# Optimization experiments

Measured on AMD Instinct MI355X. Metric: run time of the kernel, lower is better.

The kernel has to match this reference:

```python
import jax, jax.numpy as jnp
import numpy as np
from jax import lax

PATCH_SIZE = 7
NEIGH_SIZE = 9
SIGMA = 2.0
EPS = 1e-05


def _gaussian_kernel(sigma, sz):
    mid = sz // 2
    ax = np.arange(sz) - mid
    g = np.exp(-(ax[:, None] ** 2 + ax[None, :] ** 2) / (2.0 * sigma ** 2)) / (2.0 * np.pi * sigma ** 2)
    return g.astype(np.float32)


KERNEL = jnp.asarray(_gaussian_kernel(SIGMA, PATCH_SIZE))[None, None]  # (1,1,7,7)

_half = NEIGH_SIZE // 2
SHIFTS = jnp.asarray(
    [(x, y) for x in range(-_half, NEIGH_SIZE - _half)
     for y in range(-_half, NEIGH_SIZE - _half) if (x, y) != (0, 0)],
    dtype=jnp.int32)  # (80, 2) — xshift outer loop, yshift inner, matching torch order
SHIFTS4 = jnp.asarray([(-1, 0), (1, 0), (0, -1), (0, 1)], dtype=jnp.int32)


def _translate(img, tx, ty):
    # Faithful to torch affine_grid + grid_sample(nearest, zeros, align_corners=False):
    # a 'translation' of tx in normalized coords samples input at pixel j + tx*W/2.
    # H, W even and tx, ty integers -> exact integer pixel shifts, zero padding.
    H, W = img.shape
    px = jnp.arange(W) + tx * (W // 2)
    py = jnp.arange(H) + ty * (H // 2)
    mask = ((py >= 0) & (py < H))[:, None] & ((px >= 0) & (px < W))[None, :]
    out = img[jnp.clip(py, 0, H - 1)[:, None], jnp.clip(px, 0, W - 1)[None, :]]
    return jnp.where(mask, out, jnp.zeros((), img.dtype))


def _blur(x):
    # x: (N, H, W); conv2d with gaussian kernel, stride 1, padding 3 (same for 7x7)
    y = lax.conv_general_dilated(x[:, None], KERNEL, (1, 1), [(3, 3), (3, 3)],
                                 dimension_numbers=('NCHW', 'OIHW', 'NCHW'))
    return y[:, 0]


def _dp_batch(img2d, shifts):
    # Dp for a batch of shifts: shift, diff, square, gaussian blur
    shifted = jax.vmap(lambda s: _translate(img2d, s[0], s[1]))(shifts)  # (N,H,W)
    return _blur((img2d[None] - shifted) ** 2)


def setup_inputs() -> dict:
    key = jax.random.key(0)
    k1, k2 = jax.random.split(key)
    image1 = jax.random.normal(k1, (1, 1, 1024, 1024), dtype=jnp.float32)
    image2 = jax.random.normal(k2, (1, 1, 1024, 1024), dtype=jnp.float32)
    return {"image1": image1, "image2": image2}


def reference(image1, image2):
    img1 = image1[0, 0]  # (H, W)
    img2 = image2[0, 0]
    H, W = img1.shape
    reduce_size = (PATCH_SIZE + NEIGH_SIZE - 2) // 2  # = 7
    # Vimg: average of 4 single-pixel-neighborhood Dp's on image1, + eps
    Vimg = _dp_batch(img1, SHIFTS4).sum(axis=0) / 4.0 + EPS  # (H, W)
    # 80-shift MIND responses on image2
    D2 = _dp_batch(img2, SHIFTS)  # (80, H, W)
    mind = jnp.exp(-D2 / Vimg[None])
    # torch slices: dim1 end index is (C - reduce_size) = 1-7 = -6 -> H-6;
    # dim2 end index is (H - reduce_size). Replicated exactly (H == W).
    out = mind[:, reduce_size:H + 1 - reduce_size, reduce_size:H - reduce_size]
    mx = jnp.max(out, axis=0)
    return jnp.mean(out / mx[None])
```

## Files before the change

### kernel.cpp

```cpp
#include <hip/hip_runtime.h>
#include <cmath>

#define IMG_W 1024
#define SROWS 22
#define SCOLS 70

struct GK { float gh[7]; float gv[7]; };

__device__ __forceinline__ float4 pointwise(const float* __restrict__ img1,
                                            const float* __restrict__ img2,
                                            int sr, int sc)
{
    const int srp = sr ^ 512;
    const int scp = sc ^ 512;
    const float a  = img2[sr  * IMG_W + sc ];
    const float b  = img2[sr  * IMG_W + scp];
    const float cc = img2[srp * IMG_W + sc ];
    const float d  = img2[srp * IMG_W + scp];
    const float u  = img1[sr  * IMG_W + sc ];
    const float ub = img1[sr  * IMG_W + scp];
    const float uc = img1[srp * IMG_W + sc ];
    const float a2 = a * a;
    const float tb = a - b, tc = a - cc, td = a - d;
    const float su = u - ub, sv = u - uc;
    float4 f;
    f.x = fmaf(tb, tb, -a2);
    f.y = fmaf(tc, tc, -a2);
    f.z = fmaf(td, td, -a2);
    f.w = fmaf(u, u + u, fmaf(su, su, sv * sv));
    return f;
}

__global__ __launch_bounds__(256)
void mind_tile(const float* __restrict__ img1, const float* __restrict__ img2,
               float* __restrict__ partials, GK gk)
{
    __shared__ float4 s1[SROWS * SCOLS];

    const int tx  = (int)threadIdx.x;
    const int ty  = (int)threadIdx.y;
    const int tid = ty * 64 + tx;
    const int bx  = (int)blockIdx.x ^ 7;
    const int by  = (int)blockIdx.y ^ 31;
    const int x0  = 7 + 64 * bx;
    const int y0  = 7 + 16 * by;

    #pragma unroll
    for (int k = 0; k < 6; ++k) {
        const int e = tid + 256 * k;
        if (e < SROWS * 64) {
            const int r = e >> 6, c = e & 63;
            const int sr = min(y0 - 3 + r, 1023);
            const int sc = min(x0 - 3 + c, 1023);
            s1[r * SCOLS + c] = pointwise(img1, img2, sr, sc);
        }
    }
    {
        const int r = tid >> 3, c6 = tid & 7;
        if (r < SROWS && c6 < 6) {
            const int sr = min(y0 - 3 + r, 1023);
            const int sc = min(x0 + 61 + c6, 1023);
            s1[r * SCOLS + 64 + c6] = pointwise(img1, img2, sr, sc);
        }
    }
    __syncthreads();

    const bool xs = (x0 - 3 <= 511) && (x0 + 66 >= 512);
    const bool ys = (y0 - 3 <= 511) && (y0 + 18 >= 512);
    const bool xok = (x0 + tx <= 1016);
    float tsum = 0.f;

    if (!xs && !ys) {
        float Px[4] = {0,0,0,0}, Py[4] = {0,0,0,0}, Pd[4] = {0,0,0,0}, V4[4] = {0,0,0,0};
        #pragma unroll
        for (int r = 0; r < 10; ++r) {
            const float4* __restrict__ row = &s1[(4 * ty + r) * SCOLS + tx];
            float hH = 0, hV = 0, hD = 0, hU = 0;
            #pragma unroll
            for (int kx = 0; kx < 7; ++kx) {
                const float4 g = row[kx];
                hH = fmaf(gk.gh[kx], g.x, hH);
                hV = fmaf(gk.gh[kx], g.y, hV);
                hD = fmaf(gk.gh[kx], g.z, hD);
                hU = fmaf(gk.gh[kx], g.w, hU);
            }
            #pragma unroll
            for (int o = 0; o < 4; ++o) {
                if (r - o >= 0 && r - o <= 6) {
                    const float g = gk.gv[r - o];
                    Px[o] = fmaf(g, hH, Px[o]);
                    Py[o] = fmaf(g, hV, Py[o]);
                    Pd[o] = fmaf(g, hD, Pd[o]);
                    V4[o] = fmaf(g, hU, V4[o]);
                }
            }
        }
        #pragma unroll
        for (int o = 0; o < 4; ++o) {
            const float V = fmaf(V4[o], 0.25f, 1e-5f);
            const float invV = 1.0f / V;
            float M = fminf(0.f, Px[o]);
            M = fminf(M, Py[o]); M = fminf(M, Pd[o]);
            const float pix = 77.f * __expf(M * invV)
                + __expf((M - Px[o]) * invV)
                + __expf((M - Py[o]) * invV)
                + __expf((M - Pd[o]) * invV);
            const bool ok = xok && (y0 + 4 * ty + o <= 1017);
            tsum += ok ? pix : 0.f;
        }
    } else {
        float glx[7], ghx[7];
        #pragma unroll
        for (int kx = 0; kx < 7; ++kx) {
            const bool lo = (((x0 - 3 + tx + kx) & 512) == 0);
            glx[kx] = lo ? gk.gh[kx] : 0.f;
            ghx[kx] = lo ? 0.f : gk.gh[kx];
        }
        float Ph[4]  = {0,0,0,0}, Qh[4]  = {0,0,0,0}, Pv[4] = {0,0,0,0}, Qv[4] = {0,0,0,0};
        float Ppp[4] = {0,0,0,0}, Ppm[4] = {0,0,0,0}, Pmp[4] = {0,0,0,0}, Pmm[4] = {0,0,0,0};
        float V4[4]  = {0,0,0,0};
        #pragma unroll
        for (int r = 0; r < 10; ++r) {
            const float4* __restrict__ row = &s1[(4 * ty + r) * SCOLS + tx];
            float hHlo = 0, hHhi = 0, hV = 0, hDlo = 0, hDhi = 0, hU = 0;
            #pragma unroll
            for (int kx = 0; kx < 7; ++kx) {
                const float4 g = row[kx];
                hHlo = fmaf(glx[kx],   g.x, hHlo);
                hHhi = fmaf(ghx[kx],   g.x, hHhi);
                hV   = fmaf(gk.gh[kx], g.y, hV);
                hDlo = fmaf(glx[kx],   g.z, hDlo);
                hDhi = fmaf(ghx[kx],   g.z, hDhi);
                hU   = fmaf(gk.gh[kx], g.w, hU);
            }
            const bool ylo = (((y0 + 4 * ty - 3 + r) & 512) == 0);
            #pragma unroll
            for (int o = 0; o < 4; ++o) {
                if (r - o >= 0 && r - o <= 6) {
                    const float g  = gk.gv[r - o];
                    const float wl = ylo ? g : 0.f;
                    const float wh = ylo ? 0.f : g;
                    Ph [o] = fmaf(g,  hHlo, Ph [o]);
                    Qh [o] = fmaf(g,  hHhi, Qh [o]);
                    Pv [o] = fmaf(wl, hV,   Pv [o]);
                    Qv [o] = fmaf(wh, hV,   Qv [o]);
                    Ppp[o] = fmaf(wl, hDlo, Ppp[o]);
                    Ppm[o] = fmaf(wh, hDlo, Ppm[o]);
                    Pmp[o] = fmaf(wl, hDhi, Pmp[o]);
                    Pmm[o] = fmaf(wh, hDhi, Pmm[o]);
                    V4 [o] = fmaf(g,  hU,   V4 [o]);
                }
            }
        }
        #pragma unroll
        for (int o = 0; o < 4; ++o) {
            const float V = fmaf(V4[o], 0.25f, 1e-5f);
            const float invV = 1.0f / V;
            float M = fminf(0.f, Ph[o]);
            M = fminf(M, Qh[o]);  M = fminf(M, Pv[o]);  M = fminf(M, Qv[o]);
            M = fminf(M, Ppp[o]); M = fminf(M, Pmp[o]); M = fminf(M, Ppm[o]); M = fminf(M, Pmm[o]);
            const float pix = 72.f * __expf(M * invV)
                + __expf((M - Ph [o]) * invV) + __expf((M - Qh [o]) * invV)
                + __expf((M - Pv [o]) * invV) + __expf((M - Qv [o]) * invV)
                + __expf((M - Ppp[o]) * invV) + __expf((M - Pmp[o]) * invV)
                + __expf((M - Ppm[o]) * invV) + __expf((M - Pmm[o]) * invV);
            const bool ok = xok && (y0 + 4 * ty + o <= 1017);
            tsum += ok ? pix : 0.f;
        }
    }

    #pragma unroll
    for (int off = 32; off > 0; off >>= 1)
        tsum += __shfl_down(tsum, off, 64);
    __shared__ float wsum[4];
    if (tx == 0) wsum[ty] = tsum;
    __syncthreads();
    if (tid == 0)
        partials[(int)blockIdx.y * gridDim.x + (int)blockIdx.x]
            = wsum[0] + wsum[1] + wsum[2] + wsum[3];
}

__global__ __launch_bounds__(256)
void mind_reduce(const float* __restrict__ partials, float* __restrict__ out)
{
    float s = 0.f;
    #pragma unroll
    for (int k = 0; k < 4; ++k)
        s += partials[(int)threadIdx.x + 256 * k];
    double d = (double)s;
    #pragma unroll
    for (int off = 32; off > 0; off >>= 1)
        d += __shfl_down(d, off, 64);
    __shared__ double sm[4];
    const int lane = (int)threadIdx.x & 63, wid = (int)threadIdx.x >> 6;
    if (lane == 0) sm[wid] = d;
    __syncthreads();
    if (threadIdx.x == 0)
        out[0] = (float)((sm[0] + sm[1] + sm[2] + sm[3]) / 81688800.0);
}

extern "C" void kernel_launch(void* const* d_in, const int* in_sizes, int n_in,
                              void* d_out, int out_size, void* d_ws, size_t ws_size,
                              hipStream_t stream) {
    const float* img1 = (const float*)d_in[0];
    const float* img2 = (const float*)d_in[1];
    float* out = (float*)d_out;
    float* partials = (float*)d_ws;

    GK gk;
    for (int i = 0; i < 7; ++i) {
        const double d = i - 3;
        gk.gh[i] = (float)std::exp(-(d * d) / 8.0);
        gk.gv[i] = (float)(std::exp(-(d * d) / 8.0) / (8.0 * M_PI));
    }

    dim3 block(64, 4);
    dim3 grid(16, 64);
    mind_tile<<<grid, block, 0, stream>>>(img1, img2, partials, gk);
    mind_reduce<<<1, 256, 0, stream>>>(partials, out);
}
```

Baseline: 71.43 us.

## Enlarge row tile to 24 rows per block and vectorize staging loads

```diff
diff --git a/kernel.cpp b/kernel.cpp
--- a/kernel.cpp
+++ b/kernel.cpp
@@ -2,34 +2,11 @@
 #include <cmath>
 
 #define IMG_W 1024
-#define SROWS 22
+#define TROWS 24
+#define SROWS 30
 #define SCOLS 70
 
 struct GK { float gh[7]; float gv[7]; };
-
-__device__ __forceinline__ float4 pointwise(const float* __restrict__ img1,
-                                            const float* __restrict__ img2,
-                                            int sr, int sc)
-{
-    const int srp = sr ^ 512;
-    const int scp = sc ^ 512;
-    const float a  = img2[sr  * IMG_W + sc ];
-    const float b  = img2[sr  * IMG_W + scp];
-    const float cc = img2[srp * IMG_W + sc ];
-    const float d  = img2[srp * IMG_W + scp];
-    const float u  = img1[sr  * IMG_W + sc ];
-    const float ub = img1[sr  * IMG_W + scp];
-    const float uc = img1[srp * IMG_W + sc ];
-    const float a2 = a * a;
-    const float tb = a - b, tc = a - cc, td = a - d;
-    const float su = u - ub, sv = u - uc;
-    float4 f;
-    f.x = fmaf(tb, tb, -a2);
-    f.y = fmaf(tc, tc, -a2);
-    f.z = fmaf(td, td, -a2);
-    f.w = fmaf(u, u + u, fmaf(su, su, sv * sv));
-    return f;
-}
 
 __global__ __launch_bounds__(256)
 void mind_tile(const float* __restrict__ img1, const float* __restrict__ img2,
@@ -40,41 +17,82 @@
     const int tx  = (int)threadIdx.x;
     const int ty  = (int)threadIdx.y;
     const int tid = ty * 64 + tx;
-    const int bx  = (int)blockIdx.x ^ 7;
-    const int by  = (int)blockIdx.y ^ 31;
-    const int x0  = 7 + 64 * bx;
-    const int y0  = 7 + 16 * by;
-
-    #pragma unroll
-    for (int k = 0; k < 6; ++k) {
-        const int e = tid + 256 * k;
-        if (e < SROWS * 64) {
-            const int r = e >> 6, c = e & 63;
+    const int x0  = 7 + 64 * (int)blockIdx.x;
+    const int y0  = 7 + TROWS * (int)blockIdx.y;
+
+    #pragma unroll
+    for (int k = 0; k < 2; ++k) {
+        const int j = tid + 256 * k;
+        if (j < SROWS * 16) {
+            const int r  = j >> 4;
+            const int cg = (j & 15) << 2;
             const int sr = min(y0 - 3 + r, 1023);
-            const int sc = min(x0 - 3 + c, 1023);
-            s1[r * SCOLS + c] = pointwise(img1, img2, sr, sc);
+            const int srp = sr ^ 512;
+            const int sc = min(x0 - 3 + cg, 1020);
+            const int scp = sc ^ 512;
+            const float4 a  = *(const float4*)(img2 + sr  * IMG_W + sc );
+            const float4 b  = *(const float4*)(img2 + sr  * IMG_W + scp);
+            const float4 c  = *(const float4*)(img2 + srp * IMG_W + sc );
+            const float4 d  = *(const float4*)(img2 + srp * IMG_W + scp);
+            const float4 u  = *(const float4*)(img1 + sr  * IMG_W + sc );
+            const float4 ub = *(const float4*)(img1 + sr  * IMG_W + scp);
+            const float4 uc = *(const float4*)(img1 + srp * IMG_W + sc );
+            const float* ap = (const float*)&a;  const float* bp = (const float*)&b;
+            const float* cp = (const float*)&c;  const float* dp = (const float*)&d;
+            const float* up = (const float*)&u;  const float* ubp = (const float*)&ub;
+            const float* ucp = (const float*)&uc;
+            #pragma unroll
+            for (int i = 0; i < 4; ++i) {
+                const float a2 = ap[i] * ap[i];
+                const float tb = ap[i] - bp[i], tc = ap[i] - cp[i], td = ap[i] - dp[i];
+                const float su = up[i] - ubp[i], sv = up[i] - ucp[i];
+                float4 f;
+                f.x = fmaf(tb, tb, -a2);
+                f.y = fmaf(tc, tc, -a2);
+                f.z = fmaf(td, td, -a2);
+                f.w = fmaf(up[i], up[i] + up[i], fmaf(su, su, sv * sv));
+                s1[r * SCOLS + cg + i] = f;
+            }
         }
     }
     {
         const int r = tid >> 3, c6 = tid & 7;
         if (r < SROWS && c6 < 6) {
             const int sr = min(y0 - 3 + r, 1023);
+            const int srp = sr ^ 512;
             const int sc = min(x0 + 61 + c6, 1023);
-            s1[r * SCOLS + 64 + c6] = pointwise(img1, img2, sr, sc);
+            const int scp = sc ^ 512;
+            const float a  = img2[sr  * IMG_W + sc ];
+            const float b  = img2[sr  * IMG_W + scp];
+            const float c  = img2[srp * IMG_W + sc ];
+            const float d  = img2[srp * IMG_W + scp];
+            const float u  = img1[sr  * IMG_W + sc ];
+            const float ub = img1[sr  * IMG_W + scp];
+            const float uc = img1[srp * IMG_W + sc ];
+            const float a2 = a * a;
+            const float tb = a - b, tc = a - c, td = a - d;
+            const float su = u - ub, sv = u - uc;
+            float4 f;
+            f.x = fmaf(tb, tb, -a2);
+            f.y = fmaf(tc, tc, -a2);
+            f.z = fmaf(td, td, -a2);
+            f.w = fmaf(u, u + u, fmaf(su, su, sv * sv));
+            s1[r * SCOLS + 64 + c6] = f;
         }
     }
     __syncthreads();
 
     const bool xs = (x0 - 3 <= 511) && (x0 + 66 >= 512);
-    const bool ys = (y0 - 3 <= 511) && (y0 + 18 >= 512);
+    const bool ys = (y0 - 3 <= 511) && (y0 + 26 >= 512);
     const bool xok = (x0 + tx <= 1016);
     float tsum = 0.f;
 
     if (!xs && !ys) {
-        float Px[4] = {0,0,0,0}, Py[4] = {0,0,0,0}, Pd[4] = {0,0,0,0}, V4[4] = {0,0,0,0};
-        #pragma unroll
-        for (int r = 0; r < 10; ++r) {
-            const float4* __restrict__ row = &s1[(4 * ty + r) * SCOLS + tx];
+        float Px[6] = {0,0,0,0,0,0}, Py[6] = {0,0,0,0,0,0},
+              Pd[6] = {0,0,0,0,0,0}, V4[6] = {0,0,0,0,0,0};
+        #pragma unroll
+        for (int r = 0; r < 12; ++r) {
+            const float4* __restrict__ row = &s1[(6 * ty + r) * SCOLS + tx];
             float hH = 0, hV = 0, hD = 0, hU = 0;
             #pragma unroll
             for (int kx = 0; kx < 7; ++kx) {
@@ -85,7 +103,7 @@
                 hU = fmaf(gk.gh[kx], g.w, hU);
             }
             #pragma unroll
-            for (int o = 0; o < 4; ++o) {
+            for (int o = 0; o < 6; ++o) {
                 if (r - o >= 0 && r - o <= 6) {
                     const float g = gk.gv[r - o];
                     Px[o] = fmaf(g, hH, Px[o]);
@@ -96,7 +114,7 @@
             }
         }
         #pragma unroll
-        for (int o = 0; o < 4; ++o) {
+        for (int o = 0; o < 6; ++o) {
             const float V = fmaf(V4[o], 0.25f, 1e-5f);
             const float invV = 1.0f / V;
             float M = fminf(0.f, Px[o]);
@@ -105,7 +123,7 @@
                 + __expf((M - Px[o]) * invV)
                 + __expf((M - Py[o]) * invV)
                 + __expf((M - Pd[o]) * invV);
-            const bool ok = xok && (y0 + 4 * ty + o <= 1017);
+            const bool ok = xok && (y0 + 6 * ty + o <= 1017);
             tsum += ok ? pix : 0.f;
         }
     } else {
@@ -116,12 +134,14 @@
             glx[kx] = lo ? gk.gh[kx] : 0.f;
             ghx[kx] = lo ? 0.f : gk.gh[kx];
         }
-        float Ph[4]  = {0,0,0,0}, Qh[4]  = {0,0,0,0}, Pv[4] = {0,0,0,0}, Qv[4] = {0,0,0,0};
-        float Ppp[4] = {0,0,0,0}, Ppm[4] = {0,0,0,0}, Pmp[4] = {0,0,0,0}, Pmm[4] = {0,0,0,0};
-        float V4[4]  = {0,0,0,0};
-        #pragma unroll
-        for (int r = 0; r < 10; ++r) {
-            const float4* __restrict__ row = &s1[(4 * ty + r) * SCOLS + tx];
+        float Ph[6]  = {0,0,0,0,0,0}, Qh[6]  = {0,0,0,0,0,0};
+        float Pv[6]  = {0,0,0,0,0,0}, Qv[6]  = {0,0,0,0,0,0};
+        float Ppp[6] = {0,0,0,0,0,0}, Ppm[6] = {0,0,0,0,0,0};
+        float Pmp[6] = {0,0,0,0,0,0}, Pmm[6] = {0,0,0,0,0,0};
+        float V4[6]  = {0,0,0,0,0,0};
+        #pragma unroll
+        for (int r = 0; r < 12; ++r) {
+            const float4* __restrict__ row = &s1[(6 * ty + r) * SCOLS + tx];
             float hHlo = 0, hHhi = 0, hV = 0, hDlo = 0, hDhi = 0, hU = 0;
             #pragma unroll
             for (int kx = 0; kx < 7; ++kx) {
@@ -133,9 +153,9 @@
                 hDhi = fmaf(ghx[kx],   g.z, hDhi);
                 hU   = fmaf(gk.gh[kx], g.w, hU);
             }
-            const bool ylo = (((y0 + 4 * ty - 3 + r) & 512) == 0);
-            #pragma unroll
-            for (int o = 0; o < 4; ++o) {
+            const bool ylo = (((y0 + 6 * ty - 3 + r) & 512) == 0);
+            #pragma unroll
+            for (int o = 0; o < 6; ++o) {
                 if (r - o >= 0 && r - o <= 6) {
                     const float g  = gk.gv[r - o];
                     const float wl = ylo ? g : 0.f;
@@ -153,7 +173,7 @@
             }
         }
         #pragma unroll
-        for (int o = 0; o < 4; ++o) {
+        for (int o = 0; o < 6; ++o) {
             const float V = fmaf(V4[o], 0.25f, 1e-5f);
             const float invV = 1.0f / V;
             float M = fminf(0.f, Ph[o]);
@@ -164,7 +184,7 @@
                 + __expf((M - Pv [o]) * invV) + __expf((M - Qv [o]) * invV)
                 + __expf((M - Ppp[o]) * invV) + __expf((M - Pmp[o]) * invV)
                 + __expf((M - Ppm[o]) * invV) + __expf((M - Pmm[o]) * invV);
-            const bool ok = xok && (y0 + 4 * ty + o <= 1017);
+            const bool ok = xok && (y0 + 6 * ty + o <= 1017);
             tsum += ok ? pix : 0.f;
         }
     }
@@ -181,12 +201,14 @@
 }
 
 __global__ __launch_bounds__(256)
-void mind_reduce(const float* __restrict__ partials, float* __restrict__ out)
+void mind_reduce(const float* __restrict__ partials, int n, float* __restrict__ out)
 {
     float s = 0.f;
     #pragma unroll
-    for (int k = 0; k < 4; ++k)
-        s += partials[(int)threadIdx.x + 256 * k];
+    for (int k = 0; k < 3; ++k) {
+        const int i = (int)threadIdx.x + 256 * k;
+        s += (i < n) ? partials[i] : 0.f;
+    }
     double d = (double)s;
     #pragma unroll
     for (int off = 32; off > 0; off >>= 1)
@@ -215,7 +237,7 @@
     }
 
     dim3 block(64, 4);
-    dim3 grid(16, 64);
+    dim3 grid(16, 43);
     mind_tile<<<grid, block, 0, stream>>>(img1, img2, partials, gk);
-    mind_reduce<<<1, 256, 0, stream>>>(partials, out);
+    mind_reduce<<<1, 256, 0, stream>>>(partials, 16 * 43, out);
 }
```

After: 71.41 us. No clear change (-0.0%).
